# Optimization experiments

Hardware: AMD Instinct MI355X
Metric: run time of the kernel (lower is better)

Reference implementation:

```python
import jax, jax.numpy as jnp
import numpy as np

B, S, H, NH = 2, 2048, 1024, 16
HD = H // NH  # head_dim = 64
ROPE_BASE = 10000.0


def _rope(x):
    # x: [B, NH, S, HD]; LLaMA-style half-split rotary embedding
    s, d = x.shape[2], x.shape[3]
    inv_freq = 1.0 / (ROPE_BASE ** (jnp.arange(0, d, 2, dtype=jnp.float32) / d))  # [d/2]
    ang = jnp.arange(s, dtype=jnp.float32)[:, None] * inv_freq[None, :]            # [S, d/2]
    cos, sin = jnp.cos(ang), jnp.sin(ang)
    x1, x2 = x[..., : d // 2], x[..., d // 2:]
    return jnp.concatenate([x1 * cos - x2 * sin, x1 * sin + x2 * cos], axis=-1)


def setup_inputs() -> dict:
    key = jax.random.key(0)
    ks = jax.random.split(key, 9)
    hidden_states = jax.random.normal(ks[0], (B, S, H), dtype=jnp.float32)
    # causal mask: True = attend
    causal = jnp.tril(jnp.ones((S, S), dtype=bool))
    attention_mask = jnp.broadcast_to(causal[None, None, :, :], (B, 1, S, S))
    std = 0.02
    wq = jax.random.normal(ks[1], (H, NH * HD), dtype=jnp.float32) * std
    wk = jax.random.normal(ks[2], (H, NH * HD), dtype=jnp.float32) * std
    wv = jax.random.normal(ks[3], (H, NH * HD), dtype=jnp.float32) * std
    wo = jax.random.normal(ks[4], (NH * HD, H), dtype=jnp.float32) * std
    bq = jnp.zeros((NH * HD,), dtype=jnp.float32)
    bk = jnp.zeros((NH * HD,), dtype=jnp.float32)
    bv = jnp.zeros((NH * HD,), dtype=jnp.float32)
    bo = jnp.zeros((H,), dtype=jnp.float32)
    return {"hidden_states": hidden_states, "attention_mask": attention_mask,
            "wq": wq, "bq": bq, "wk": wk, "bk": bk, "wv": wv, "bv": bv,
            "wo": wo, "bo": bo}


def _split_heads(x):
    b, s, _ = x.shape
    return jnp.transpose(x.reshape(b, s, NH, HD), (0, 2, 1, 3))


def reference(hidden_states, attention_mask, wq, bq, wk, bk, wv, bv, wo, bo):
    q = _split_heads(hidden_states @ wq + bq)  # [B,NH,S,HD]
    k = _split_heads(hidden_states @ wk + bk)
    v = _split_heads(hidden_states @ wv + bv)
    q = _rope(q)
    k = _rope(k)
    scores = jnp.einsum('bhqd,bhkd->bhqk', q, k) / jnp.sqrt(jnp.float32(HD))
    scores = jnp.where(attention_mask, scores, jnp.float32(-1e9))
    weights = jax.nn.softmax(scores, axis=-1)
    attn = jnp.einsum('bhqk,bhkv->bhqv', weights, v)  # [B,NH,S,HD]
    attn = jnp.transpose(attn, (0, 2, 1, 3)).reshape(hidden_states.shape[0], attn.shape[2], H)
    return attn @ wo + bo
```

## Files before the change

### kernel.cpp

```cpp
#include <hip/hip_runtime.h>
#include <math.h>

typedef short bf16x8 __attribute__((ext_vector_type(8)));
typedef short bf16x4 __attribute__((ext_vector_type(4)));
typedef float f32x4  __attribute__((ext_vector_type(4)));

__device__ __forceinline__ unsigned short f2bf(float f) {
    union { float f; unsigned u; } v; v.f = f;
    unsigned r = v.u + 0x7FFFu + ((v.u >> 16) & 1u);
    return (unsigned short)(r >> 16);
}

__device__ __forceinline__ unsigned cvt_pk_bf16(float a, float b) {
    unsigned r;
    asm("v_cvt_pk_bf16_f32 %0, %1, %2" : "=v"(r) : "v"(a), "v"(b));
    return r;
}

#define GLDS16(gp, lp) __builtin_amdgcn_global_load_lds( \
    (const __attribute__((address_space(1))) void*)(gp), \
    (__attribute__((address_space(3))) void*)(lp), 16, 0, 0)


__device__ const unsigned XT[20] = {
    59399u, 63559u, 67719u, 71879u,
    30725u, 34885u, 39045u,
    10243u, 14403u,
    133121u,
    42758u, 46910u, 51062u, 55214u,
    18180u, 22332u,
    26228u,
    1538u, 5682u,
    132096u
};

__global__ __launch_bounds__(256)
void prep(const float* __restrict__ X, unsigned short* __restrict__ Xb,
          const float* __restrict__ w0, const float* __restrict__ w1,
          const float* __restrict__ w2, const float* __restrict__ w3,
          unsigned short* o0, unsigned short* o1,
          unsigned short* o2, unsigned short* o3)
{
    const int z = blockIdx.z;
    if (z >= 4) {
        const int lb = (z - 4) * 256 + blockIdx.y * 16 + blockIdx.x;
        const size_t t = (size_t)lb * 256 + threadIdx.x;
        const float4 a = *(const float4*)(X + t * 8);
        const float4 b = *(const float4*)(X + t * 8 + 4);
        unsigned short u[8] = { f2bf(a.x), f2bf(a.y), f2bf(a.z), f2bf(a.w),
                                f2bf(b.x), f2bf(b.y), f2bf(b.z), f2bf(b.w) };
        *(int4*)(Xb + t * 8) = *(int4*)u;
        return;
    }
    const float* W; unsigned short* O;
    switch (z) {
        case 0: W = w0; O = o0; break;
        case 1: W = w1; O = o1; break;
        case 2: W = w2; O = o2; break;
        default: W = w3; O = o3; break;
    }
    __shared__ float T[64][65];
    const int tid = threadIdx.x;
    const int n0 = blockIdx.x * 64, k0 = blockIdx.y * 64;
    #pragma unroll
    for (int i = 0; i < 4; i++) {
        const int k = (tid >> 4) + i * 16, n4 = (tid & 15) * 4;
        const float4 v = *(const float4*)(W + (size_t)(k0 + k) * 1024 + n0 + n4);
        T[k][n4] = v.x; T[k][n4+1] = v.y; T[k][n4+2] = v.z; T[k][n4+3] = v.w;
    }
    __syncthreads();
    if (z == 3) {
        #pragma unroll
        for (int i = 0; i < 4; i++) {
            const int n = (tid >> 4) + i * 16, k4 = (tid & 15) * 4;
            unsigned short u[4];
            #pragma unroll
            for (int j = 0; j < 4; j++) {
                const int q = k4 + j;
                const int p = (q & 3) * 16 + (q >> 2);
                const int d = (p & 3) * 16 + (p >> 2);
                u[j] = f2bf(T[d][n]);
            }
            *(int2*)(O + (size_t)(n0 + n) * 1024 + k0 + k4) = *(int2*)u;
        }
    } else {
        #pragma unroll
        for (int i = 0; i < 4; i++) {
            const int n = (tid >> 4) + i * 16, k4 = (tid & 15) * 4;
            unsigned short u[4] = { f2bf(T[k4][n]), f2bf(T[k4+1][n]),
                                    f2bf(T[k4+2][n]), f2bf(T[k4+3][n]) };
            *(int2*)(O + (size_t)(n0 + n) * 1024 + k0 + k4) = *(int2*)u;
        }
    }
}

__global__ __launch_bounds__(256)
void qkv_gemm(const unsigned short* __restrict__ Xb,
              const unsigned short* __restrict__ Wtq, const unsigned short* __restrict__ Wtk,
              const unsigned short* __restrict__ Wtv,
              const float* __restrict__ bq, const float* __restrict__ bk,
              const float* __restrict__ bv,
              unsigned short* __restrict__ Qb, unsigned short* __restrict__ Kb,
              unsigned short* __restrict__ Vtb)
{
    const unsigned short* Wt; const float* bias; unsigned short* Out;
    const int z = blockIdx.z;
    if (z == 0)      { Wt = Wtq; bias = bq; Out = Qb; }
    else if (z == 1) { Wt = Wtk; bias = bk; Out = Kb; }
    else             { Wt = Wtv; bias = bv; Out = Vtb; }

    __shared__ unsigned short Sh[16384];
    unsigned short* T = Sh;

    const int tid = threadIdx.x, lane = tid & 63, w = tid >> 6;
    const int quad = lane >> 4, c = lane & 15;
    const int wr = w >> 1, wc = w & 1;
    const int m0 = blockIdx.x * 128, n0 = blockIdx.y * 128;
    const int srow = lane >> 2;
    const int scol = ((lane & 3) ^ ((lane >> 3) & 3)) * 8;
    const int sA = (quad ^ ((c >> 1) & 3)) * 8;

    f32x4 acc[4][4];
    #pragma unroll
    for (int i = 0; i < 4; i++)
        #pragma unroll
        for (int j = 0; j < 4; j++) acc[i][j] = (f32x4){0.f, 0.f, 0.f, 0.f};

    #pragma unroll
    for (int j = 0; j < 2; j++) {
        const int r = w * 32 + j * 16;
        GLDS16(Xb + (size_t)(m0 + r + srow) * 1024 + 0 + scol, &Sh[r * 32]);
        GLDS16(Wt + (size_t)(n0 + r + srow) * 1024 + 0 + scol, &Sh[4096 + r * 32]);
    }
    __syncthreads();

    int cur = 0;
    for (int t = 0; t < 32; ++t) {
        if (t + 1 < 32) {
            const int kn = (t + 1) * 32;
            unsigned short* An = Sh + (cur ^ 1) * 8192;
            unsigned short* Bn = An + 4096;
            #pragma unroll
            for (int j = 0; j < 2; j++) {
                const int r = w * 32 + j * 16;
                GLDS16(Xb + (size_t)(m0 + r + srow) * 1024 + kn + scol, &An[r * 32]);
                GLDS16(Wt + (size_t)(n0 + r + srow) * 1024 + kn + scol, &Bn[r * 32]);
            }
        }
        const unsigned short* As = Sh + cur * 8192;
        const unsigned short* Bs = As + 4096;
        bf16x8 af[4], bf[4];
        #pragma unroll
        for (int rt = 0; rt < 4; rt++)
            af[rt] = *(const bf16x8*)&As[(wr * 64 + rt * 16 + c) * 32 + sA];
        #pragma unroll
        for (int nt = 0; nt < 4; nt++)
            bf[nt] = *(const bf16x8*)&Bs[(wc * 64 + nt * 16 + c) * 32 + sA];
        #pragma unroll
        for (int rt = 0; rt < 4; rt++)
            #pragma unroll
            for (int nt = 0; nt < 4; nt++)
                acc[rt][nt] = __builtin_amdgcn_mfma_f32_16x16x32_bf16(af[rt], bf[nt], acc[rt][nt], 0, 0, 0);
        __syncthreads();
        cur ^= 1;
    }

    float bv4[4];
    #pragma unroll
    for (int nt = 0; nt < 4; nt++) bv4[nt] = bias[n0 + wc * 64 + nt * 16 + c];

    if (z == 2) {
        const int b = m0 >> 11, sb = m0 & 2047;
        const int hgbase = n0 >> 6;
        #pragma unroll
        for (int h = 0; h < 2; h++) {
            if (wc == h) {
                #pragma unroll
                for (int rt = 0; rt < 4; rt++)
                    #pragma unroll
                    for (int reg = 0; reg < 4; reg++) {
                        const int s = wr * 64 + rt * 16 + quad * 4 + reg;
                        unsigned short u[4];
                        #pragma unroll
                        for (int nt = 0; nt < 4; nt++)
                            u[nt] = f2bf(acc[rt][nt][reg] + bv4[nt]);
                        *(int2*)&T[s * 72 + c * 4] = *(int2*)u;
                    }
            }
            __syncthreads();
            const int p = tid >> 2, s8 = (tid & 3) * 32;
            unsigned short* dstb = Vtb + ((size_t)(b * 16 + hgbase + h) * 64 + p) * 2048 + sb;
            #pragma unroll
            for (int jj = 0; jj < 32; jj += 8) {
                unsigned short u[8];
                #pragma unroll
                for (int j = 0; j < 8; j++) u[j] = T[(s8 + jj + j) * 72 + p];
                *(int4*)(dstb + s8 + jj) = *(int4*)u;
            }
            __syncthreads();
        }
        return;
    }

    const float kLn = 9.210340371976184f / 32.0f;
    const float TWO_PI_INV = 0.15915494309189535f;
    const float rv0 = expf(-(float)c * kLn) * TWO_PI_INV;
    const float rv1 = expf(-(float)(c + 16) * kLn) * TWO_PI_INV;
    const float qscale = (z == 0) ? 0.125f : 1.0f;

    #pragma unroll
    for (int rt = 0; rt < 4; rt++) {
        #pragma unroll
        for (int reg = 0; reg < 4; reg++) {
            const int m = m0 + wr * 64 + rt * 16 + quad * 4 + reg;
            const int b = m >> 11, s = m & 2047;
            float x0 = acc[rt][0][reg] + bv4[0];
            float x1 = acc[rt][1][reg] + bv4[1];
            float x2 = acc[rt][2][reg] + bv4[2];
            float x3 = acc[rt][3][reg] + bv4[3];
            float r0 = (float)s * rv0;  r0 -= floorf(r0);
            float r1 = (float)s * rv1;  r1 -= floorf(r1);
            const float sn0 = __builtin_amdgcn_sinf(r0);
            const float cs0 = __builtin_amdgcn_cosf(r0);
            const float sn1 = __builtin_amdgcn_sinf(r1);
            const float cs1 = __builtin_amdgcn_cosf(r1);
            const float y0 = (x0 * cs0 - x2 * sn0) * qscale;
            const float y2 = (x0 * sn0 + x2 * cs0) * qscale;
            const float y1 = (x1 * cs1 - x3 * sn1) * qscale;
            const float y3 = (x1 * sn1 + x3 * cs1) * qscale;
            const int h = (n0 + wc * 64) >> 6;
            unsigned short u[4] = { f2bf(y0), f2bf(y1), f2bf(y2), f2bf(y3) };
            unsigned short* dst = Out + ((size_t)(b * 16 + h) * 2048 + s) * 64;
            *(int2*)(dst + c * 4) = *(int2*)u;
        }
    }
}

__global__ __launch_bounds__(256)
void out_gemm(const unsigned short* __restrict__ Ab, const unsigned short* __restrict__ Wto,
              const float* __restrict__ bo, float* __restrict__ Out)
{
    __shared__ unsigned short As[64 * 32];
    __shared__ unsigned short Bs[128 * 32];
    const int tid = threadIdx.x, lane = tid & 63, w = tid >> 6;
    const int quad = lane >> 4, c = lane & 15;
    const int wr = w >> 1, wc = w & 1;
    const int m0 = blockIdx.x * 64, n0 = blockIdx.y * 128;
    const int srow = lane >> 2, scol = (lane & 3) * 8;

    f32x4 acc[2][4];
    #pragma unroll
    for (int i = 0; i < 2; i++)
        #pragma unroll
        for (int j = 0; j < 4; j++) acc[i][j] = (f32x4){0.f, 0.f, 0.f, 0.f};

    for (int k0 = 0; k0 < 1024; k0 += 32) {
        {
            const int r = w * 16;
            GLDS16(Ab + (size_t)(m0 + r + srow) * 1024 + k0 + scol, &As[r * 32]);
        }
        #pragma unroll
        for (int j = 0; j < 2; j++) {
            const int r = w * 32 + j * 16;
            GLDS16(Wto + (size_t)(n0 + r + srow) * 1024 + k0 + scol, &Bs[r * 32]);
        }
        __syncthreads();
        bf16x8 af[2], bf[4];
        #pragma unroll
        for (int rt = 0; rt < 2; rt++)
            af[rt] = *(const bf16x8*)&As[(wr * 32 + rt * 16 + c) * 32 + quad * 8];
        #pragma unroll
        for (int nt = 0; nt < 4; nt++)
            bf[nt] = *(const bf16x8*)&Bs[(wc * 64 + nt * 16 + c) * 32 + quad * 8];
        #pragma unroll
        for (int rt = 0; rt < 2; rt++)
            #pragma unroll
            for (int nt = 0; nt < 4; nt++)
                acc[rt][nt] = __builtin_amdgcn_mfma_f32_16x16x32_bf16(af[rt], bf[nt], acc[rt][nt], 0, 0, 0);
        __syncthreads();
    }
    #pragma unroll
    for (int rt = 0; rt < 2; rt++) {
        #pragma unroll
        for (int reg = 0; reg < 4; reg++) {
            const int m = m0 + wr * 32 + rt * 16 + quad * 4 + reg;
            #pragma unroll
            for (int nt = 0; nt < 4; nt++) {
                const int n = n0 + wc * 64 + nt * 16 + c;
                Out[(size_t)m * 1024 + n] = acc[rt][nt][reg] + bo[n];
            }
        }
    }
}

__global__ __launch_bounds__(512)
void attn_part(const unsigned short* __restrict__ Qb, const unsigned short* __restrict__ Kb,
               const unsigned short* __restrict__ Vtb, unsigned short* __restrict__ Ab,
               float* __restrict__ Opart, float* __restrict__ Lpart)
{
    __shared__ unsigned short Ks[64 * 72];
    __shared__ unsigned short Vs[64 * 72];

    const int tid = threadIdx.x, w = tid >> 6, lane = tid & 63;
    const int quad = lane >> 4, c = lane & 15;
    const int bh = blockIdx.y;
    const unsigned e = XT[blockIdx.x];
    const int i     = e & 7;
    const int start = (e >> 3) & 31;
    const int len   = (e >> 8) & 15;
    const int slot  = (e >> 12) & 31;
    const bool complete = (e >> 17) & 1;
    const int q0 = i * 256;
    const size_t base = (size_t)bh * 2048 * 64;

    bf16x8 on;
    #pragma unroll
    for (int ii = 0; ii < 8; ii++) on[ii] = (short)0x3F80;

    const int qbase = q0 + w * 32;
    const size_t qoffA = base + (size_t)(qbase + c) * 64;
    const size_t qoffB = base + (size_t)(qbase + 16 + c) * 64;
    const bf16x8 qfA0 = *(const bf16x8*)(Qb + qoffA + quad * 8);
    const bf16x8 qfA1 = *(const bf16x8*)(Qb + qoffA + 32 + quad * 8);
    const bf16x8 qfB0 = *(const bf16x8*)(Qb + qoffB + quad * 8);
    const bf16x8 qfB1 = *(const bf16x8*)(Qb + qoffB + 32 + quad * 8);

    f32x4 OA[4], OB[4], OsA, OsB;
    OsA = (f32x4){0.f, 0.f, 0.f, 0.f};
    OsB = (f32x4){0.f, 0.f, 0.f, 0.f};
    #pragma unroll
    for (int nt = 0; nt < 4; nt++) { OA[nt] = OsA; OB[nt] = OsA; }

    const int rs = tid >> 3, c8 = (tid & 7) * 8;

    int k0 = start * 64;
    int4 kreg = *(const int4*)(Kb  + base + (size_t)(k0 + rs) * 64 + c8);
    int4 vreg = *(const int4*)(Vtb + base + (size_t)rs * 2048 + k0 + c8);

    union P8 { bf16x8 v8; unsigned wd[4]; };
    union V8 { bf16x8 v8; bf16x4 v4[2]; };

    for (int t = 0; t < len; t++, k0 += 64) {
        *(int4*)&Ks[(size_t)rs * 72 + c8] = kreg;
        *(int4*)&Vs[(size_t)rs * 72 + c8] = vreg;
        __syncthreads();

        if (t + 1 < len) {
            const int kn = k0 + 64;
            kreg = *(const int4*)(Kb  + base + (size_t)(kn + rs) * 64 + c8);
            vreg = *(const int4*)(Vtb + base + (size_t)rs * 2048 + kn + c8);
        }

        if (k0 <= qbase + 31) {
            const int qrowA = qbase + c;
            const int qrowB = qbase + 16 + c;
            const bool nmA = (k0 + 63) > qbase;
            const bool nmB = (k0 + 63) > (qbase + 16);
            P8 paA0, paA1, paB0, paB1;
            __builtin_amdgcn_s_setprio(1);
            #pragma unroll
            for (int nt = 0; nt < 4; nt++) {
                const bf16x8 kf0 = *(const bf16x8*)&Ks[(nt * 16 + c) * 72 + quad * 8];
                const bf16x8 kf1 = *(const bf16x8*)&Ks[(nt * 16 + c) * 72 + 32 + quad * 8];
                f32x4 sA = (f32x4){0.f, 0.f, 0.f, 0.f};
                f32x4 sB = sA;
                sA = __builtin_amdgcn_mfma_f32_16x16x32_bf16(kf0, qfA0, sA, 0, 0, 0);
                sA = __builtin_amdgcn_mfma_f32_16x16x32_bf16(kf1, qfA1, sA, 0, 0, 0);
                sB = __builtin_amdgcn_mfma_f32_16x16x32_bf16(kf0, qfB0, sB, 0, 0, 0);
                sB = __builtin_amdgcn_mfma_f32_16x16x32_bf16(kf1, qfB1, sB, 0, 0, 0);
                const int keyb = k0 + nt * 16 + quad * 4;
                float pA[4], pB[4];
                #pragma unroll
                for (int reg = 0; reg < 4; reg++) {
                    float va = __expf(sA[reg]);
                    if (nmA && (keyb + reg > qrowA)) va = 0.f;
                    pA[reg] = va;
                    float vb = __expf(sB[reg]);
                    if (nmB && (keyb + reg > qrowB)) vb = 0.f;
                    pB[reg] = vb;
                }
                const unsigned waA = cvt_pk_bf16(pA[0], pA[1]);
                const unsigned wbA = cvt_pk_bf16(pA[2], pA[3]);
                const unsigned waB = cvt_pk_bf16(pB[0], pB[1]);
                const unsigned wbB = cvt_pk_bf16(pB[2], pB[3]);
                if (nt < 2) {
                    paA0.wd[2 * nt] = waA;     paA0.wd[2 * nt + 1] = wbA;
                    paB0.wd[2 * nt] = waB;     paB0.wd[2 * nt + 1] = wbB;
                } else {
                    paA1.wd[2 * (nt-2)] = waA; paA1.wd[2 * (nt-2) + 1] = wbA;
                    paB1.wd[2 * (nt-2)] = waB; paB1.wd[2 * (nt-2) + 1] = wbB;
                }
            }

            #pragma unroll
            for (int nt = 0; nt < 4; nt++) {
                const int pr = (nt * 16 + c) * 72 + 4 * quad;
                V8 vb0, vb1;
                vb0.v4[0] = *(const bf16x4*)&Vs[pr];
                vb0.v4[1] = *(const bf16x4*)&Vs[pr + 16];
                vb1.v4[0] = *(const bf16x4*)&Vs[pr + 32];
                vb1.v4[1] = *(const bf16x4*)&Vs[pr + 48];
                OA[nt] = __builtin_amdgcn_mfma_f32_16x16x32_bf16(paA0.v8, vb0.v8, OA[nt], 0, 0, 0);
                OA[nt] = __builtin_amdgcn_mfma_f32_16x16x32_bf16(paA1.v8, vb1.v8, OA[nt], 0, 0, 0);
                OB[nt] = __builtin_amdgcn_mfma_f32_16x16x32_bf16(paB0.v8, vb0.v8, OB[nt], 0, 0, 0);
                OB[nt] = __builtin_amdgcn_mfma_f32_16x16x32_bf16(paB1.v8, vb1.v8, OB[nt], 0, 0, 0);
            }
            OsA = __builtin_amdgcn_mfma_f32_16x16x32_bf16(paA0.v8, on, OsA, 0, 0, 0);
            OsA = __builtin_amdgcn_mfma_f32_16x16x32_bf16(paA1.v8, on, OsA, 0, 0, 0);
            OsB = __builtin_amdgcn_mfma_f32_16x16x32_bf16(paB0.v8, on, OsB, 0, 0, 0);
            OsB = __builtin_amdgcn_mfma_f32_16x16x32_bf16(paB1.v8, on, OsB, 0, 0, 0);
            __builtin_amdgcn_s_setprio(0);
        }
        __syncthreads();
    }

    if (complete) {
        const int b = bh >> 4, h = bh & 15;
        #pragma unroll
        for (int reg = 0; reg < 4; reg++) {
            const float invA = 1.0f / OsA[reg];
            const int qA = qbase + quad * 4 + reg;
            unsigned short uA[4];
            #pragma unroll
            for (int nt = 0; nt < 4; nt++) uA[nt] = f2bf(OA[nt][reg] * invA);
            unsigned short* dA = Ab + ((size_t)(b * 2048 + qA)) * 1024 + h * 64;
            *(int2*)(dA + c * 4) = *(int2*)uA;

            const float invB = 1.0f / OsB[reg];
            const int qB = qbase + 16 + quad * 4 + reg;
            unsigned short uB[4];
            #pragma unroll
            for (int nt = 0; nt < 4; nt++) uB[nt] = f2bf(OB[nt][reg] * invB);
            unsigned short* dB = Ab + ((size_t)(b * 2048 + qB)) * 1024 + h * 64;
            *(int2*)(dB + c * 4) = *(int2*)uB;
        }
    } else {
        float* Op = Opart + ((size_t)bh * 18 + slot) * 16384;
        float* Lp = Lpart + ((size_t)bh * 18 + slot) * 256;
        #pragma unroll
        for (int reg = 0; reg < 4; reg++) {
            const int rowA = w * 32 + quad * 4 + reg;
            float4 oA = make_float4(OA[0][reg], OA[1][reg], OA[2][reg], OA[3][reg]);
            *(float4*)(Op + (size_t)rowA * 64 + c * 4) = oA;
            if (c == 0) Lp[rowA] = OsA[reg];

            const int rowB = rowA + 16;
            float4 oB = make_float4(OB[0][reg], OB[1][reg], OB[2][reg], OB[3][reg]);
            *(float4*)(Op + (size_t)rowB * 64 + c * 4) = oB;
            if (c == 0) Lp[rowB] = OsB[reg];
        }
    }
}

__global__ __launch_bounds__(256)
void attn_combine(const float* __restrict__ Opart, const float* __restrict__ Lpart,
                  unsigned short* __restrict__ Ab)
{
    const int tid = threadIdx.x;
    const int j = blockIdx.x, bh = blockIdx.y;
    const int i = 2 + (j >> 1), half = j & 1;
    const int sb = (i < 4) ? 2 * (i - 2) : ((i < 6) ? 3 * i - 8 : 4 * i - 14);
    const int n  = (i < 4) ? 2 : ((i < 6) ? 3 : 4);
    const int q0 = i * 256 + half * 128;
    const size_t s0 = ((size_t)bh * 18 + sb) * 16384 + (size_t)half * 128 * 64;
    const size_t l0 = ((size_t)bh * 18 + sb) * 256 + half * 128;

    __shared__ float linv[128];
    if (tid < 128) {
        float l = 0.f;
        for (int s = 0; s < n; s++) l += Lpart[l0 + (size_t)s * 256 + tid];
        linv[tid] = 1.0f / l;
    }
    __syncthreads();

    const int row = tid >> 1, col0 = (tid & 1) * 32;
    const float inv = linv[row];
    const int b = bh >> 4, h = bh & 15;
    const int q = q0 + row;
    unsigned short* dst = Ab + ((size_t)(b * 2048 + q)) * 1024 + h * 64 + col0;
    #pragma unroll
    for (int c4 = 0; c4 < 32; c4 += 4) {
        float4 a = *(const float4*)(Opart + s0 + (size_t)row * 64 + col0 + c4);
        for (int s = 1; s < n; s++) {
            const float4 bb = *(const float4*)(Opart + s0 + (size_t)s * 16384 + (size_t)row * 64 + col0 + c4);
            a.x += bb.x; a.y += bb.y; a.z += bb.z; a.w += bb.w;
        }
        dst[c4 + 0] = f2bf(a.x * inv);
        dst[c4 + 1] = f2bf(a.y * inv);
        dst[c4 + 2] = f2bf(a.z * inv);
        dst[c4 + 3] = f2bf(a.w * inv);
    }
}

extern "C" void kernel_launch(void* const* d_in, const int* in_sizes, int n_in,
                              void* d_out, int out_size, void* d_ws, size_t ws_size,
                              hipStream_t stream)
{
    const float* X  = (const float*)d_in[0];
    const float* wq = (const float*)d_in[2];
    const float* bq = (const float*)d_in[3];
    const float* wk = (const float*)d_in[4];
    const float* bk = (const float*)d_in[5];
    const float* wv = (const float*)d_in[6];
    const float* bv = (const float*)d_in[7];
    const float* wo = (const float*)d_in[8];
    const float* bo = (const float*)d_in[9];

    unsigned short* ws = (unsigned short*)d_ws;
    const size_t M1 = 1024 * 1024;
    unsigned short* Xb  = ws;
    unsigned short* Wtq = Xb  + 4 * M1;
    unsigned short* Wtk = Wtq + M1;
    unsigned short* Wtv = Wtk + M1;
    unsigned short* Wto = Wtv + M1;
    unsigned short* Qb  = Wto + M1;
    unsigned short* Kb  = Qb  + 4 * M1;
    unsigned short* Vtb = Kb  + 4 * M1;
    unsigned short* Ab  = Vtb + 4 * M1;
    float* Opart = (float*)(Ab + 4 * M1);
    float* Lpart = Opart + (size_t)32 * 18 * 16384;

    prep        <<<dim3(16, 16, 12), 256, 0, stream>>>(X, Xb, wq, wk, wv, wo,
                                                       Wtq, Wtk, Wtv, Wto);
    qkv_gemm    <<<dim3(32, 8, 3), 256, 0, stream>>>(Xb, Wtq, Wtk, Wtv, bq, bk, bv,
                                                     Qb, Kb, Vtb);
    attn_part   <<<dim3(20, 32), 512, 0, stream>>>(Qb, Kb, Vtb, Ab, Opart, Lpart);
    attn_combine<<<dim3(12, 32), 256, 0, stream>>>(Opart, Lpart, Ab);
    out_gemm    <<<dim3(64, 8), 256, 0, stream>>>(Ab, Wto, bo, (float*)d_out);
}
```

Baseline: 229.8 us.

## Double-buffer LDS in out_gemm and attention, add XOR swizzle

```diff
diff --git a/kernel.cpp b/kernel.cpp
--- a/kernel.cpp
+++ b/kernel.cpp
@@ -240,13 +240,14 @@
 void out_gemm(const unsigned short* __restrict__ Ab, const unsigned short* __restrict__ Wto,
               const float* __restrict__ bo, float* __restrict__ Out)
 {
-    __shared__ unsigned short As[64 * 32];
-    __shared__ unsigned short Bs[128 * 32];
+    __shared__ unsigned short Sh[12288];
     const int tid = threadIdx.x, lane = tid & 63, w = tid >> 6;
     const int quad = lane >> 4, c = lane & 15;
     const int wr = w >> 1, wc = w & 1;
     const int m0 = blockIdx.x * 64, n0 = blockIdx.y * 128;
-    const int srow = lane >> 2, scol = (lane & 3) * 8;
+    const int srow = lane >> 2;
+    const int scol = ((lane & 3) ^ ((lane >> 3) & 3)) * 8;
+    const int sA = (quad ^ ((c >> 1) & 3)) * 8;
 
     f32x4 acc[2][4];
     #pragma unroll
@@ -254,30 +255,43 @@
         #pragma unroll
         for (int j = 0; j < 4; j++) acc[i][j] = (f32x4){0.f, 0.f, 0.f, 0.f};
 
-    for (int k0 = 0; k0 < 1024; k0 += 32) {
-        {
-            const int r = w * 16;
-            GLDS16(Ab + (size_t)(m0 + r + srow) * 1024 + k0 + scol, &As[r * 32]);
-        }
-        #pragma unroll
-        for (int j = 0; j < 2; j++) {
-            const int r = w * 32 + j * 16;
-            GLDS16(Wto + (size_t)(n0 + r + srow) * 1024 + k0 + scol, &Bs[r * 32]);
-        }
-        __syncthreads();
+    GLDS16(Ab + (size_t)(m0 + w * 16 + srow) * 1024 + 0 + scol, &Sh[(w * 16) * 32]);
+    #pragma unroll
+    for (int j = 0; j < 2; j++) {
+        const int r = w * 32 + j * 16;
+        GLDS16(Wto + (size_t)(n0 + r + srow) * 1024 + 0 + scol, &Sh[2048 + r * 32]);
+    }
+    __syncthreads();
+
+    int cur = 0;
+    for (int t = 0; t < 32; ++t) {
+        if (t + 1 < 32) {
+            const int kn = (t + 1) * 32;
+            unsigned short* An = Sh + (cur ^ 1) * 6144;
+            unsigned short* Bn = An + 2048;
+            GLDS16(Ab + (size_t)(m0 + w * 16 + srow) * 1024 + kn + scol, &An[(w * 16) * 32]);
+            #pragma unroll
+            for (int j = 0; j < 2; j++) {
+                const int r = w * 32 + j * 16;
+                GLDS16(Wto + (size_t)(n0 + r + srow) * 1024 + kn + scol, &Bn[r * 32]);
+            }
+        }
+        const unsigned short* As = Sh + cur * 6144;
+        const unsigned short* Bs = As + 2048;
         bf16x8 af[2], bf[4];
         #pragma unroll
         for (int rt = 0; rt < 2; rt++)
-            af[rt] = *(const bf16x8*)&As[(wr * 32 + rt * 16 + c) * 32 + quad * 8];
+            af[rt] = *(const bf16x8*)&As[(wr * 32 + rt * 16 + c) * 32 + sA];
         #pragma unroll
         for (int nt = 0; nt < 4; nt++)
-            bf[nt] = *(const bf16x8*)&Bs[(wc * 64 + nt * 16 + c) * 32 + quad * 8];
+            bf[nt] = *(const bf16x8*)&Bs[(wc * 64 + nt * 16 + c) * 32 + sA];
         #pragma unroll
         for (int rt = 0; rt < 2; rt++)
             #pragma unroll
             for (int nt = 0; nt < 4; nt++)
                 acc[rt][nt] = __builtin_amdgcn_mfma_f32_16x16x32_bf16(af[rt], bf[nt], acc[rt][nt], 0, 0, 0);
         __syncthreads();
+        cur ^= 1;
     }
     #pragma unroll
     for (int rt = 0; rt < 2; rt++) {
@@ -298,8 +312,8 @@
                const unsigned short* __restrict__ Vtb, unsigned short* __restrict__ Ab,
                float* __restrict__ Opart, float* __restrict__ Lpart)
 {
-    __shared__ unsigned short Ks[64 * 72];
-    __shared__ unsigned short Vs[64 * 72];
+    __shared__ unsigned short Ks[2][64 * 72];
+    __shared__ unsigned short Vs[2][64 * 72];
 
     const int tid = threadIdx.x, w = tid >> 6, lane = tid & 63;
     const int quad = lane >> 4, c = lane & 15;
@@ -340,9 +354,10 @@
     union P8 { bf16x8 v8; unsigned wd[4]; };
     union V8 { bf16x8 v8; bf16x4 v4[2]; };
 
+    int cur = 0;
     for (int t = 0; t < len; t++, k0 += 64) {
-        *(int4*)&Ks[(size_t)rs * 72 + c8] = kreg;
-        *(int4*)&Vs[(size_t)rs * 72 + c8] = vreg;
+        *(int4*)&Ks[cur][(size_t)rs * 72 + c8] = kreg;
+        *(int4*)&Vs[cur][(size_t)rs * 72 + c8] = vreg;
         __syncthreads();
 
         if (t + 1 < len) {
@@ -360,8 +375,8 @@
             __builtin_amdgcn_s_setprio(1);
             #pragma unroll
             for (int nt = 0; nt < 4; nt++) {
-                const bf16x8 kf0 = *(const bf16x8*)&Ks[(nt * 16 + c) * 72 + quad * 8];
-                const bf16x8 kf1 = *(const bf16x8*)&Ks[(nt * 16 + c) * 72 + 32 + quad * 8];
+                const bf16x8 kf0 = *(const bf16x8*)&Ks[cur][(nt * 16 + c) * 72 + quad * 8];
+                const bf16x8 kf1 = *(const bf16x8*)&Ks[cur][(nt * 16 + c) * 72 + 32 + quad * 8];
                 f32x4 sA = (f32x4){0.f, 0.f, 0.f, 0.f};
                 f32x4 sB = sA;
                 sA = __builtin_amdgcn_mfma_f32_16x16x32_bf16(kf0, qfA0, sA, 0, 0, 0);
@@ -396,10 +411,10 @@
             for (int nt = 0; nt < 4; nt++) {
                 const int pr = (nt * 16 + c) * 72 + 4 * quad;
                 V8 vb0, vb1;
-                vb0.v4[0] = *(const bf16x4*)&Vs[pr];
-                vb0.v4[1] = *(const bf16x4*)&Vs[pr + 16];
-                vb1.v4[0] = *(const bf16x4*)&Vs[pr + 32];
-                vb1.v4[1] = *(const bf16x4*)&Vs[pr + 48];
+                vb0.v4[0] = *(const bf16x4*)&Vs[cur][pr];
+                vb0.v4[1] = *(const bf16x4*)&Vs[cur][pr + 16];
+                vb1.v4[0] = *(const bf16x4*)&Vs[cur][pr + 32];
+                vb1.v4[1] = *(const bf16x4*)&Vs[cur][pr + 48];
                 OA[nt] = __builtin_amdgcn_mfma_f32_16x16x32_bf16(paA0.v8, vb0.v8, OA[nt], 0, 0, 0);
                 OA[nt] = __builtin_amdgcn_mfma_f32_16x16x32_bf16(paA1.v8, vb1.v8, OA[nt], 0, 0, 0);
                 OB[nt] = __builtin_amdgcn_mfma_f32_16x16x32_bf16(paB0.v8, vb0.v8, OB[nt], 0, 0, 0);
@@ -411,7 +426,7 @@
             OsB = __builtin_amdgcn_mfma_f32_16x16x32_bf16(paB1.v8, on, OsB, 0, 0, 0);
             __builtin_amdgcn_s_setprio(0);
         }
-        __syncthreads();
+        cur ^= 1;
     }
 
     if (complete) {
```

New measurement: 231.0 us. Within noise of the previous version (+0.6%).
